# Performance work log

Measured on AMD Instinct MI355X. Metric: run time of the kernel, lower is better.

The kernel has to match this reference:

```python
import jax, jax.numpy as jnp
import numpy as np


def _conv_same(x, w, b):
    # 3x3 same-padding conv, NCHW / OIHW (matches ConvNdWithSamePadding with
    # kernel=3, stride=1, dilation=1 -> symmetric pad of 1)
    y = jax.lax.conv_general_dilated(
        x, w, window_strides=(1, 1), padding='SAME',
        dimension_numbers=('NCHW', 'OIHW', 'NCHW'))
    return y + b[None, :, None, None]


def setup_inputs() -> dict:
    key = jax.random.key(0)
    ks = jax.random.split(key, 5)
    B, A, C, H, W = 8, 6, 256, 32, 32
    x = jax.random.normal(ks[0], (B, A, C, H, W), dtype=jnp.float32)
    w_ih = jax.random.normal(ks[1], (3 * C, 2 * C, 3, 3), dtype=jnp.float32) * 0.02
    w_hh = jax.random.normal(ks[2], (3 * C, C, 3, 3), dtype=jnp.float32) * 0.02
    b_ih = jax.random.normal(ks[3], (3 * C,), dtype=jnp.float32) * 0.02
    b_hh = jax.random.normal(ks[4], (3 * C,), dtype=jnp.float32) * 0.02
    return {'x': x, 'w_ih': w_ih, 'w_hh': w_hh, 'b_ih': b_ih, 'b_hh': b_hh,
            'num_iters': 3}


def reference(x, w_ih, w_hh, b_ih, b_hh, num_iters):
    # x: [B, A, C, H, W] per-agent BEV features.
    # Each GNN iteration: message = mean of other agents' features,
    # GRU input = concat(own, message) [2C ch], hidden = own feature [C ch],
    # new feature = ConvGRU cell output.
    B, A, C, H, W = x.shape
    for _ in range(num_iters):
        # mean over the other A-1 agents, computed via total sum (vectorized)
        msg = (jnp.sum(x, axis=1, keepdims=True) - x) / (A - 1)
        inp = jnp.concatenate([x, msg], axis=2).reshape(B * A, 2 * C, H, W)
        h = x.reshape(B * A, C, H, W)
        gi = _conv_same(inp, w_ih, b_ih)   # [B*A, 3C, H, W]
        gh = _conv_same(h, w_hh, b_hh)     # [B*A, 3C, H, W]
        i_r, i_i, i_n = jnp.split(gi, 3, axis=1)
        h_r, h_i, h_n = jnp.split(gh, 3, axis=1)
        resetgate = jax.nn.sigmoid(i_r + h_r)
        inputgate = jax.nn.sigmoid(i_i + h_i)
        newgate = jnp.tanh(i_n + resetgate * h_n)
        hy = newgate + inputgate * (h - newgate)
        x = hy.reshape(B, A, C, H, W)
    return x
```

## Files before the change

### kernel.cpp

```cpp
#include <hip/hip_runtime.h>
#include <stdint.h>

typedef unsigned short u16;
typedef __attribute__((ext_vector_type(8))) short short8;
typedef __attribute__((ext_vector_type(4))) float f32x4;

__device__ __forceinline__ u16 f2bf(float f) {
  uint32_t u = __builtin_bit_cast(uint32_t, f);
  u += 0x7fffu + ((u >> 16) & 1u);
  return (u16)(u >> 16);
}

__device__ __forceinline__ void gld16(const void* g, void* l) {
  __builtin_amdgcn_global_load_lds(
      (const __attribute__((address_space(1))) void*)g,
      (__attribute__((address_space(3))) void*)l, 16, 0, 0);
}

__global__ __launch_bounds__(256) void k_wprep(const float* __restrict__ w_ih,
                                               const float* __restrict__ w_hh,
                                               u16* __restrict__ wA,
                                               u16* __restrict__ wS) {
  const int NA = 8*9*8*192*32;
  const int NS = 8*9*8*96*32;
  for (int idx = blockIdx.x*blockDim.x + threadIdx.x; idx < NA + NS;
       idx += gridDim.x*blockDim.x) {
    if (idx < NA) {
      int kk = idx & 31; int t = idx >> 5;
      int nl = t % 192; t /= 192;
      int kb = t & 7; t >>= 3;
      int tap = t % 9; int cb = t / 9;
      int g = nl >> 5, cl = nl & 31;
      int c = cb*32 + cl, ci = kb*32 + kk;
      float v;
      if (g < 3) {
        int o = g*256 + c;
        v = w_ih[(o*512 + ci)*9 + tap] - 0.2f * w_ih[(o*512 + 256 + ci)*9 + tap];
      } else {
        int o = (g-3)*256 + c;
        v = w_hh[(o*256 + ci)*9 + tap];
      }
      wA[idx] = f2bf(v);
    } else {
      int j = idx - NA;
      int kk = j & 31; int t = j >> 5;
      int nl = t % 96; t /= 96;
      int kb = t & 7; t >>= 3;
      int tap = t % 9; int cb = t / 9;
      int o = cb*96 + nl, ci = kb*32 + kk;
      wS[j] = f2bf(0.2f * w_ih[(o*512 + 256 + ci)*9 + tap]);
    }
  }
}

__global__ __launch_bounds__(256) void k_xform(const float* __restrict__ src,
                                               u16* __restrict__ xbf,
                                               u16* __restrict__ sbf) {
  __shared__ float lds[32][33];
  const int t = threadIdx.x;
  const int tx = t & 31, ty = t >> 5;
  const int p0 = blockIdx.x*32, c0 = blockIdx.y*32, b = blockIdx.z;
  const int po = t >> 3, co = (t & 7)*4;
  float ss[4] = {0.f,0.f,0.f,0.f};
  for (int a = 0; a < 6; ++a) {
    const int im = b*6 + a;
    const float* sp = src + ((size_t)im*256 + c0)*1024 + p0;
    #pragma unroll
    for (int k = 0; k < 4; ++k) {
      float v = sp[(size_t)(ty + 8*k)*1024 + tx];
      ss[k] += v;
      lds[ty + 8*k][tx] = v;
    }
    __syncthreads();
    ushort4 pk = make_ushort4(f2bf(lds[co+0][po]), f2bf(lds[co+1][po]),
                              f2bf(lds[co+2][po]), f2bf(lds[co+3][po]));
    *(ushort4*)(xbf + ((size_t)im*1024 + p0+po)*256 + c0 + co) = pk;
    __syncthreads();
  }
  #pragma unroll
  for (int k = 0; k < 4; ++k) lds[ty + 8*k][tx] = ss[k];
  __syncthreads();
  ushort4 pk = make_ushort4(f2bf(lds[co+0][po]), f2bf(lds[co+1][po]),
                            f2bf(lds[co+2][po]), f2bf(lds[co+3][po]));
  *(ushort4*)(sbf + ((size_t)b*1024 + p0+po)*256 + c0 + co) = pk;
}

template<int W, int NF, bool GATES>
__global__ __launch_bounds__(W*64, 2)
void k_conv(const u16* __restrict__ xin, const u16* __restrict__ wpre,
            float* __restrict__ gsbuf,
            const float* __restrict__ b_ih, const float* __restrict__ b_hh,
            const float* __restrict__ h_in, float* __restrict__ h_out) {
  constexpr int NT = W*64;
  constexpr int SLAB = (W+2)*32*32;
  constexpr int BBN  = NF*16*32;
  __shared__ __align__(16) u16 slab[2][SLAB];
  __shared__ __align__(16) u16 bbuf[2][BBN];

  const int tid = threadIdx.x;
  const int l  = tid & 63;
  const int w  = tid >> 6;
  const int lx = l & 15;
  const int lk = l >> 4;

  int bid = blockIdx.x;
  const int cb = bid & 7; bid >>= 3;
  constexpr int MT = 32 / W;
  const int mt = bid % MT;
  const int img = bid / MT;
  const int h0 = mt * W;

  const u16* srcimg = xin + (size_t)img * 1024 * 256;

  auto stageA = [&](int kb, int sb) {
    constexpr int TOT = (W+2)*128;
    #pragma unroll
    for (int ii = 0; ii < (TOT + NT - 1)/NT; ++ii) {
      int i = ii*NT + tid;
      if (i < TOT) {
        int p = i >> 2, ck = i & 3;
        int pr = p >> 5, pc = p & 31;
        int gr = h0 - 1 + pr;
        gr = gr < 0 ? 0 : (gr > 31 ? 31 : gr);
        int sck = ck ^ ((p >> 1) & 3);
        gld16(srcimg + (gr*32 + pc)*256 + kb*32 + sck*8, &slab[sb][i*8]);
      }
    }
  };
  auto stageB = [&](int kb, int tap, int bb) {
    constexpr int TOT = NF*64;
    const u16* wb = wpre + (size_t)((cb*9 + tap)*8 + kb) * (NF*16*32);
    #pragma unroll
    for (int ii = 0; ii < (TOT + NT - 1)/NT; ++ii) {
      int i = ii*NT + tid;
      if (i < TOT) {
        int nl = i >> 2, ck = i & 3;
        int sck = ck ^ ((nl >> 1) & 3);
        gld16(wb + nl*32 + sck*8, &bbuf[bb][i*8]);
      }
    }
  };

  f32x4 acc[2][NF];
  #pragma unroll
  for (int mi = 0; mi < 2; ++mi)
    #pragma unroll
    for (int f = 0; f < NF; ++f) acc[mi][f] = (f32x4){0.f,0.f,0.f,0.f};

  stageA(0, 0);
  stageB(0, 0, 0);
  __syncthreads();

  const int R = h0 + w;
  const int bofs = lx*32 + (lk ^ ((lx >> 1) & 3))*8;

  for (int kb = 0; kb < 8; ++kb) {
    const int sb = kb & 1;
    #pragma unroll
    for (int tap = 0; tap < 9; ++tap) {
      const int bb = (kb*9 + tap) & 1;
      if (tap < 8) {
        stageB(kb, tap+1, bb^1);
      } else if (kb < 7) {
        stageA(kb+1, sb^1);
        stageB(kb+1, 0, bb^1);
      }
      const int dy = tap/3, dx = tap%3;
      const int grow = R + dy - 1;
      const bool rowok = (grow >= 0) && (grow < 32);
      const int sr = w + dy;
      short8 a[2];
      #pragma unroll
      for (int mi = 0; mi < 2; ++mi) {
        int cc = mi*16 + lx + dx - 1;
        bool ok = rowok && (cc >= 0) && (cc < 32);
        int ccc = cc < 0 ? 0 : (cc > 31 ? 31 : cc);
        int pl = sr*32 + ccc;
        short8 av = *(const short8*)&slab[sb][pl*32 + (lk ^ ((ccc >> 1) & 3))*8];
        if (!ok) av = (short8){0,0,0,0,0,0,0,0};
        a[mi] = av;
      }
      const u16* bp = &bbuf[bb][bofs];
      #pragma unroll
      for (int f = 0; f < NF; ++f) {
        short8 bv = *(const short8*)(bp + f*512);
        acc[0][f] = __builtin_amdgcn_mfma_f32_16x16x32_bf16(a[0], bv, acc[0][f], 0, 0, 0);
        acc[1][f] = __builtin_amdgcn_mfma_f32_16x16x32_bf16(a[1], bv, acc[1][f], 0, 0, 0);
      }
      __syncthreads();
    }
  }

  if constexpr (GATES) {
    const int b = img / 6;
    const size_t imgoff = (size_t)img * 256 * 1024;
    #pragma unroll
    for (int q = 0; q < 2; ++q) {
      const int c = cb*32 + q*16 + lx;
      const float bi_r = b_ih[c], bi_i = b_ih[256+c], bi_n = b_ih[512+c];
      const float bh_r = b_hh[c], bh_i = b_hh[256+c], bh_n = b_hh[512+c];
      const float* gs0 = gsbuf + ((size_t)(b*3+0)*256 + c)*1024;
      const float* gs1 = gsbuf + ((size_t)(b*3+1)*256 + c)*1024;
      const float* gs2 = gsbuf + ((size_t)(b*3+2)*256 + c)*1024;
      const float* hip_ = h_in + imgoff + (size_t)c*1024;
      float* hop_ = h_out + imgoff + (size_t)c*1024;
      #pragma unroll
      for (int mi = 0; mi < 2; ++mi) {
        #pragma unroll
        for (int r = 0; r < 4; ++r) {
          const int pix = R*32 + mi*16 + lk*4 + r;
          float ir  = acc[mi][0+q][r]  + gs0[pix] + bi_r;
          float ii  = acc[mi][2+q][r]  + gs1[pix] + bi_i;
          float inn = acc[mi][4+q][r]  + gs2[pix] + bi_n;
          float hr  = acc[mi][6+q][r]  + bh_r;
          float hi2 = acc[mi][8+q][r]  + bh_i;
          float hn  = acc[mi][10+q][r] + bh_n;
          float rg = 1.f/(1.f + __expf(-(ir+hr)));
          float ig = 1.f/(1.f + __expf(-(ii+hi2)));
          float nx = inn + rg*hn;
          nx = nx > 20.f ? 20.f : (nx < -20.f ? -20.f : nx);
          float e2 = __expf(-2.f*nx);
          float ng = (1.f - e2)/(1.f + e2);
          float hold = hip_[pix];
          hop_[pix] = ng + ig*(hold - ng);
        }
      }
    }
  } else {
    #pragma unroll
    for (int f = 0; f < NF; ++f) {
      const int n = cb*(NF*16) + f*16 + lx;
      float* gp = gsbuf + ((size_t)img*768 + n)*1024;
      #pragma unroll
      for (int mi = 0; mi < 2; ++mi)
        #pragma unroll
        for (int r = 0; r < 4; ++r)
          gp[R*32 + mi*16 + lk*4 + r] = acc[mi][f][r];
    }
  }
}

extern "C" void kernel_launch(void* const* d_in, const int* in_sizes, int n_in,
                              void* d_out, int out_size, void* d_ws, size_t ws_size,
                              hipStream_t stream) {
  const float* x    = (const float*)d_in[0];
  const float* w_ih = (const float*)d_in[1];
  const float* w_hh = (const float*)d_in[2];
  const float* b_ih = (const float*)d_in[3];
  const float* b_hh = (const float*)d_in[4];
  float* out = (float*)d_out;

  char* ws = (char*)d_ws;
  float* m0  = (float*)(ws);
  u16*  xbf  = (u16*)(ws + 50331648);
  u16*  sbf  = (u16*)(ws + 75497472);
  float* gsb = (float*)(ws + 79691776);
  u16*  wA   = (u16*)(ws + 104857600);
  u16*  wS   = (u16*)(ws + 111935488);

  k_wprep<<<2048, 256, 0, stream>>>(w_ih, w_hh, wA, wS);

  for (int it = 0; it < 3; ++it) {
    const float* src = (it == 0) ? x : (it == 1 ? out : m0);
    float* dst = (it == 1) ? m0 : out;
    k_xform<<<dim3(32, 8, 8), 256, 0, stream>>>(src, xbf, sbf);
    k_conv<8, 6, false><<<256, 512, 0, stream>>>(sbf, wS, gsb,
                                                 nullptr, nullptr, nullptr, nullptr);
    k_conv<8, 12, true><<<1536, 512, 0, stream>>>(xbf, wA, gsb,
                                                  b_ih, b_hh, src, dst);
  }
}
```

Before: 1.508 ms.

## Retile conv waves 2x2 and triple-buffer weights with explicit vmcnt waits

Each wave now covers two rows by 16 output channels (four M tiles times GF N tiles) instead of one row by all channels, which cuts LDS B-fragment reads per MFMA. Weight staging moves to a three-deep ring prefetched two steps ahead, and slab prefetch starts one tap earlier. Per-tap __syncthreads is replaced by s_waitcnt vmcnt plus s_barrier, and MFMA sections get s_setprio. The weight prep is reordered so each wave's gate channels sit together, and the epilogue uses float4 loads and stores. Register pressure rises (96 accumulator floats), and the hand-counted waits are fragile.

```diff
diff --git a/kernel.cpp b/kernel.cpp
--- a/kernel.cpp
+++ b/kernel.cpp
@@ -15,6 +15,18 @@
   __builtin_amdgcn_global_load_lds(
       (const __attribute__((address_space(1))) void*)g,
       (__attribute__((address_space(3))) void*)l, 16, 0, 0);
+}
+
+__device__ __forceinline__ void waitv(int n) {
+  switch (n) {
+    case 0: asm volatile("s_waitcnt vmcnt(0)" ::: "memory"); break;
+    case 1: asm volatile("s_waitcnt vmcnt(1)" ::: "memory"); break;
+    case 2: asm volatile("s_waitcnt vmcnt(2)" ::: "memory"); break;
+    case 3: asm volatile("s_waitcnt vmcnt(3)" ::: "memory"); break;
+    case 4: asm volatile("s_waitcnt vmcnt(4)" ::: "memory"); break;
+    case 5: asm volatile("s_waitcnt vmcnt(5)" ::: "memory"); break;
+    default: asm volatile("s_waitcnt vmcnt(6)" ::: "memory"); break;
+  }
 }
 
 __global__ __launch_bounds__(256) void k_wprep(const float* __restrict__ w_ih,
@@ -30,8 +42,9 @@
       int nl = t % 192; t /= 192;
       int kb = t & 7; t >>= 3;
       int tap = t % 9; int cb = t / 9;
-      int g = nl >> 5, cl = nl & 31;
-      int c = cb*32 + cl, ci = kb*32 + kk;
+      int qq = nl / 96; int rr = nl % 96;
+      int g = rr >> 4, cl = rr & 15;
+      int c = cb*32 + qq*16 + cl, ci = kb*32 + kk;
       float v;
       if (g < 3) {
         int o = g*256 + c;
@@ -85,55 +98,60 @@
   *(ushort4*)(sbf + ((size_t)b*1024 + p0+po)*256 + c0 + co) = pk;
 }
 
-template<int W, int NF, bool GATES>
-__global__ __launch_bounds__(W*64, 2)
+template<int GF, bool GATES>
+__global__ __launch_bounds__(512, 2)
 void k_conv(const u16* __restrict__ xin, const u16* __restrict__ wpre,
             float* __restrict__ gsbuf,
             const float* __restrict__ b_ih, const float* __restrict__ b_hh,
             const float* __restrict__ h_in, float* __restrict__ h_out) {
-  constexpr int NT = W*64;
-  constexpr int SLAB = (W+2)*32*32;
-  constexpr int BBN  = NF*16*32;
+  constexpr int NT   = 512;
+  constexpr int SLAB = 10*32*32;
+  constexpr int BN   = 2*GF*16*32;
+  constexpr int TOTA = 10*128;
+  constexpr int TOTB = BN/8;
   __shared__ __align__(16) u16 slab[2][SLAB];
-  __shared__ __align__(16) u16 bbuf[2][BBN];
+  __shared__ __align__(16) u16 bbuf[3][BN];
 
   const int tid = threadIdx.x;
   const int l  = tid & 63;
   const int w  = tid >> 6;
   const int lx = l & 15;
   const int lk = l >> 4;
+  const int rg = w >> 1;
+  const int q  = w & 1;
 
   int bid = blockIdx.x;
   const int cb = bid & 7; bid >>= 3;
-  constexpr int MT = 32 / W;
-  const int mt = bid % MT;
-  const int img = bid / MT;
-  const int h0 = mt * W;
-
-  const u16* srcimg = xin + (size_t)img * 1024 * 256;
-
-  auto stageA = [&](int kb, int sb) {
-    constexpr int TOT = (W+2)*128;
-    #pragma unroll
-    for (int ii = 0; ii < (TOT + NT - 1)/NT; ++ii) {
+  const int mt = bid & 3;
+  const int img = bid >> 2;
+  const int h0 = mt * 8;
+
+  const u16* srcimg = xin + (size_t)img * (1024*256);
+
+  const int trf = __builtin_amdgcn_readfirstlane(tid);
+  const int myB = TOTB/NT + ((trf < (TOTB % NT)) ? 1 : 0);
+  const int myA = TOTA/NT + ((trf < (TOTA % NT)) ? 1 : 0);
+
+  auto stageA = [&](int kb, int sbuf) {
+    #pragma unroll
+    for (int ii = 0; ii < (TOTA + NT - 1)/NT; ++ii) {
       int i = ii*NT + tid;
-      if (i < TOT) {
+      if (i < TOTA) {
         int p = i >> 2, ck = i & 3;
         int pr = p >> 5, pc = p & 31;
         int gr = h0 - 1 + pr;
         gr = gr < 0 ? 0 : (gr > 31 ? 31 : gr);
         int sck = ck ^ ((p >> 1) & 3);
-        gld16(srcimg + (gr*32 + pc)*256 + kb*32 + sck*8, &slab[sb][i*8]);
+        gld16(srcimg + (gr*32 + pc)*256 + kb*32 + sck*8, &slab[sbuf][i*8]);
       }
     }
   };
   auto stageB = [&](int kb, int tap, int bb) {
-    constexpr int TOT = NF*64;
-    const u16* wb = wpre + (size_t)((cb*9 + tap)*8 + kb) * (NF*16*32);
-    #pragma unroll
-    for (int ii = 0; ii < (TOT + NT - 1)/NT; ++ii) {
+    const u16* wb = wpre + (size_t)((cb*9 + tap)*8 + kb) * BN;
+    #pragma unroll
+    for (int ii = 0; ii < (TOTB + NT - 1)/NT; ++ii) {
       int i = ii*NT + tid;
-      if (i < TOT) {
+      if (i < TOTB) {
         int nl = i >> 2, ck = i & 3;
         int sck = ck ^ ((nl >> 1) & 3);
         gld16(wb + nl*32 + sck*8, &bbuf[bb][i*8]);
@@ -141,101 +159,105 @@
     }
   };
 
-  f32x4 acc[2][NF];
+  f32x4 acc[4][GF];
   #pragma unroll
-  for (int mi = 0; mi < 2; ++mi)
-    #pragma unroll
-    for (int f = 0; f < NF; ++f) acc[mi][f] = (f32x4){0.f,0.f,0.f,0.f};
+  for (int mi = 0; mi < 4; ++mi)
+    #pragma unroll
+    for (int g = 0; g < GF; ++g) acc[mi][g] = (f32x4){0.f,0.f,0.f,0.f};
 
   stageA(0, 0);
   stageB(0, 0, 0);
-  __syncthreads();
-
-  const int R = h0 + w;
-  const int bofs = lx*32 + (lk ^ ((lx >> 1) & 3))*8;
+  stageB(0, 1, 1);
 
   for (int kb = 0; kb < 8; ++kb) {
     const int sb = kb & 1;
     #pragma unroll
     for (int tap = 0; tap < 9; ++tap) {
-      const int bb = (kb*9 + tap) & 1;
-      if (tap < 8) {
-        stageB(kb, tap+1, bb^1);
-      } else if (kb < 7) {
-        stageA(kb+1, sb^1);
-        stageB(kb+1, 0, bb^1);
-      }
+      const int tau = kb*9 + tap;
+      if (tau == 71) waitv(0);
+      else if (tap == 7 && kb < 7) waitv(myA + myB);
+      else waitv(myB);
+      __builtin_amdgcn_s_barrier();
+      __builtin_amdgcn_sched_barrier(0);
+
+      if (tap == 6 && kb < 7) stageA(kb+1, sb^1);
+      if (tau <= 69) stageB((tau+2)/9, (tau+2)%9, (tau+2)%3);
+
       const int dy = tap/3, dx = tap%3;
-      const int grow = R + dy - 1;
-      const bool rowok = (grow >= 0) && (grow < 32);
-      const int sr = w + dy;
-      short8 a[2];
-      #pragma unroll
-      for (int mi = 0; mi < 2; ++mi) {
-        int cc = mi*16 + lx + dx - 1;
-        bool ok = rowok && (cc >= 0) && (cc < 32);
-        int ccc = cc < 0 ? 0 : (cc > 31 ? 31 : cc);
-        int pl = sr*32 + ccc;
-        short8 av = *(const short8*)&slab[sb][pl*32 + (lk ^ ((ccc >> 1) & 3))*8];
+      short8 a[4];
+      #pragma unroll
+      for (int mi = 0; mi < 4; ++mi) {
+        const int grow = h0 + rg*2 + (mi>>1) + dy - 1;
+        const int cc = (mi&1)*16 + lx + dx - 1;
+        const bool ok = (grow >= 0) && (grow < 32) && (cc >= 0) && (cc < 32);
+        const int ccc = cc < 0 ? 0 : (cc > 31 ? 31 : cc);
+        const int sr = rg*2 + (mi>>1) + dy;
+        short8 av = *(const short8*)&slab[sb][(sr*32 + ccc)*32 + (lk ^ ((ccc >> 1) & 3))*8];
         if (!ok) av = (short8){0,0,0,0,0,0,0,0};
         a[mi] = av;
       }
-      const u16* bp = &bbuf[bb][bofs];
-      #pragma unroll
-      for (int f = 0; f < NF; ++f) {
-        short8 bv = *(const short8*)(bp + f*512);
-        acc[0][f] = __builtin_amdgcn_mfma_f32_16x16x32_bf16(a[0], bv, acc[0][f], 0, 0, 0);
-        acc[1][f] = __builtin_amdgcn_mfma_f32_16x16x32_bf16(a[1], bv, acc[1][f], 0, 0, 0);
-      }
-      __syncthreads();
+      const u16* bp = &bbuf[tau % 3][(q*(GF*16) + lx)*32 + (lk ^ ((lx >> 1) & 3))*8];
+      __builtin_amdgcn_s_setprio(1);
+      #pragma unroll
+      for (int g = 0; g < GF; ++g) {
+        short8 bv = *(const short8*)(bp + g*(16*32));
+        #pragma unroll
+        for (int mi = 0; mi < 4; ++mi)
+          acc[mi][g] = __builtin_amdgcn_mfma_f32_16x16x32_bf16(a[mi], bv, acc[mi][g], 0, 0, 0);
+      }
+      __builtin_amdgcn_s_setprio(0);
     }
   }
 
   if constexpr (GATES) {
     const int b = img / 6;
-    const size_t imgoff = (size_t)img * 256 * 1024;
-    #pragma unroll
-    for (int q = 0; q < 2; ++q) {
-      const int c = cb*32 + q*16 + lx;
-      const float bi_r = b_ih[c], bi_i = b_ih[256+c], bi_n = b_ih[512+c];
-      const float bh_r = b_hh[c], bh_i = b_hh[256+c], bh_n = b_hh[512+c];
-      const float* gs0 = gsbuf + ((size_t)(b*3+0)*256 + c)*1024;
-      const float* gs1 = gsbuf + ((size_t)(b*3+1)*256 + c)*1024;
-      const float* gs2 = gsbuf + ((size_t)(b*3+2)*256 + c)*1024;
-      const float* hip_ = h_in + imgoff + (size_t)c*1024;
-      float* hop_ = h_out + imgoff + (size_t)c*1024;
-      #pragma unroll
-      for (int mi = 0; mi < 2; ++mi) {
-        #pragma unroll
-        for (int r = 0; r < 4; ++r) {
-          const int pix = R*32 + mi*16 + lk*4 + r;
-          float ir  = acc[mi][0+q][r]  + gs0[pix] + bi_r;
-          float ii  = acc[mi][2+q][r]  + gs1[pix] + bi_i;
-          float inn = acc[mi][4+q][r]  + gs2[pix] + bi_n;
-          float hr  = acc[mi][6+q][r]  + bh_r;
-          float hi2 = acc[mi][8+q][r]  + bh_i;
-          float hn  = acc[mi][10+q][r] + bh_n;
-          float rg = 1.f/(1.f + __expf(-(ir+hr)));
-          float ig = 1.f/(1.f + __expf(-(ii+hi2)));
-          float nx = inn + rg*hn;
-          nx = nx > 20.f ? 20.f : (nx < -20.f ? -20.f : nx);
-          float e2 = __expf(-2.f*nx);
-          float ng = (1.f - e2)/(1.f + e2);
-          float hold = hip_[pix];
-          hop_[pix] = ng + ig*(hold - ng);
-        }
-      }
+    const int c = cb*32 + q*16 + lx;
+    const float bir = b_ih[c],  bii = b_ih[256+c], bin_ = b_ih[512+c];
+    const float bhr = b_hh[c],  bhi = b_hh[256+c], bhn  = b_hh[512+c];
+    const float* gs0 = gsbuf + ((size_t)(b*3+0)*256 + c)*1024;
+    const float* gs1 = gsbuf + ((size_t)(b*3+1)*256 + c)*1024;
+    const float* gs2 = gsbuf + ((size_t)(b*3+2)*256 + c)*1024;
+    const float* hp  = h_in  + ((size_t)img*256 + c)*1024;
+    float*       op  = h_out + ((size_t)img*256 + c)*1024;
+    #pragma unroll
+    for (int mi = 0; mi < 4; ++mi) {
+      const int R = h0 + rg*2 + (mi>>1);
+      const int pix = R*32 + (mi&1)*16 + lk*4;
+      float4 v0 = *(const float4*)(gs0 + pix);
+      float4 v1 = *(const float4*)(gs1 + pix);
+      float4 v2 = *(const float4*)(gs2 + pix);
+      float4 hv = *(const float4*)(hp + pix);
+      float4 o;
+      #pragma unroll
+      for (int r = 0; r < 4; ++r) {
+        float ir  = acc[mi][0][r] + (&v0.x)[r] + bir;
+        float ii  = acc[mi][1][r] + (&v1.x)[r] + bii;
+        float inn = acc[mi][2][r] + (&v2.x)[r] + bin_;
+        float hr  = acc[mi][3][r] + bhr;
+        float hi2 = acc[mi][4][r] + bhi;
+        float hn  = acc[mi][5][r] + bhn;
+        float rgt = 1.f/(1.f + __expf(-(ir+hr)));
+        float igt = 1.f/(1.f + __expf(-(ii+hi2)));
+        float nx = inn + rgt*hn;
+        nx = nx > 20.f ? 20.f : (nx < -20.f ? -20.f : nx);
+        float e2 = __expf(-2.f*nx);
+        float ng = (1.f - e2)/(1.f + e2);
+        (&o.x)[r] = ng + igt*((&hv.x)[r] - ng);
+      }
+      *(float4*)(op + pix) = o;
     }
   } else {
     #pragma unroll
-    for (int f = 0; f < NF; ++f) {
-      const int n = cb*(NF*16) + f*16 + lx;
+    for (int g = 0; g < GF; ++g) {
+      const int n = cb*(2*GF*16) + q*(GF*16) + g*16 + lx;
       float* gp = gsbuf + ((size_t)img*768 + n)*1024;
       #pragma unroll
-      for (int mi = 0; mi < 2; ++mi)
-        #pragma unroll
-        for (int r = 0; r < 4; ++r)
-          gp[R*32 + mi*16 + lk*4 + r] = acc[mi][f][r];
+      for (int mi = 0; mi < 4; ++mi) {
+        const int R = h0 + rg*2 + (mi>>1);
+        const int pix = R*32 + (mi&1)*16 + lk*4;
+        *(float4*)(gp + pix) = make_float4(acc[mi][g][0], acc[mi][g][1],
+                                           acc[mi][g][2], acc[mi][g][3]);
+      }
     }
   }
 }
@@ -264,9 +286,9 @@
     const float* src = (it == 0) ? x : (it == 1 ? out : m0);
     float* dst = (it == 1) ? m0 : out;
     k_xform<<<dim3(32, 8, 8), 256, 0, stream>>>(src, xbf, sbf);
-    k_conv<8, 6, false><<<256, 512, 0, stream>>>(sbf, wS, gsb,
-                                                 nullptr, nullptr, nullptr, nullptr);
-    k_conv<8, 12, true><<<1536, 512, 0, stream>>>(xbf, wA, gsb,
-                                                  b_ih, b_hh, src, dst);
-  }
-}
+    k_conv<3, false><<<256, 512, 0, stream>>>(sbf, wS, gsb,
+                                              nullptr, nullptr, nullptr, nullptr);
+    k_conv<6, true><<<1536, 512, 0, stream>>>(xbf, wA, gsb,
+                                              b_ih, b_hh, src, dst);
+  }
+}
```

Measured after the change: 1.541 ms. 1.02x slower.
